# Kernel optimization log

Measured on AMD Instinct MI355X. Metric: run time of the kernel, lower is better.

## Reference

```python
import jax, jax.numpy as jnp
import numpy as np

B, N, M, D = 4096, 50, 64, 64   # batch, fields_dim, embedding_dim, product_layer_dim
V = 100000                      # features_dim (vocab)
HIDDEN = [512, 256, 128]
BN_EPS = 1e-3


def setup_inputs() -> dict:
    key = jax.random.key(0)
    ks = jax.random.split(key, 32)
    inp = {
        "feature_value": jax.random.uniform(ks[0], (B, N), dtype=jnp.float32),
        "embedding_index": jax.random.randint(ks[1], (B, N), 0, V, dtype=jnp.int32),
        "emb_table": jax.random.uniform(ks[2], (V, M), dtype=jnp.float32, minval=-0.05, maxval=0.05),
        "linear_signals": jax.random.normal(ks[3], (D, N, M), dtype=jnp.float32) * 0.05,
        "theta": jax.random.normal(ks[4], (D, N), dtype=jnp.float32) * 0.05,
        "quad_w": jax.random.normal(ks[5], (D, M, M), dtype=jnp.float32) * 0.05,
    }
    in_dim = 3 * D  # concat(l_z, l_p_inner, l_p_outer)
    dims = [in_dim] + HIDDEN
    k = 6
    for i, (di, do) in enumerate(zip(dims[:-1], dims[1:])):
        inp[f"W{i}"] = jax.random.normal(ks[k], (di, do), dtype=jnp.float32) * (1.0 / np.sqrt(di)); k += 1
        inp[f"b{i}"] = jnp.zeros((do,), dtype=jnp.float32)
        inp[f"g{i}"] = jnp.ones((do,), dtype=jnp.float32)
        inp[f"be{i}"] = jnp.zeros((do,), dtype=jnp.float32)
        inp[f"m{i}"] = jnp.zeros((do,), dtype=jnp.float32)
        inp[f"v{i}"] = jnp.ones((do,), dtype=jnp.float32)
    inp["Wout"] = jax.random.normal(ks[k], (HIDDEN[-1], 1), dtype=jnp.float32) * (1.0 / np.sqrt(HIDDEN[-1]))
    inp["bout"] = jnp.zeros((1,), dtype=jnp.float32)
    return inp


def _pnn_forward(feature_value, embedding_index, emb_table, linear_signals, theta, quad_w,
                 dense_params, Wout, bout):
    # features: [b, n, m] = embedding lookup scaled per-field by feature_value
    feats = emb_table[embedding_index] * feature_value[:, :, None]
    # linear signal: 'bnm,dnm->bd'
    l_z = jnp.einsum('bnm,dnm->bd', feats, linear_signals)
    # ipnn branch: delta = 'dn,bnm->bdnm'; l_p = sum delta*delta over (n,m)
    # algebraic rewrite (same math): sum_n theta_dn^2 * (sum_m feats_bnm^2)
    l_p_in = jnp.einsum('bn,dn->bd', jnp.sum(feats * feats, axis=2), theta * theta)
    # opnn branch: p = outer(sum_feats, sum_feats); 'bmn,dmn->bd'
    s = jnp.sum(feats, axis=1)  # [b, m]
    l_p_out = jnp.einsum('bm,dmn,bn->bd', s, quad_w, s)
    x = jnp.concatenate([l_z, l_p_in, l_p_out], axis=1)  # [b, 3d]
    # MLP stack: Dense -> BatchNorm(inference) -> ReLU (dropout is identity at eval)
    for (W, b, g, be, mu, var) in dense_params:
        x = x @ W + b
        x = g * (x - mu) * jax.lax.rsqrt(var + BN_EPS) + be
        x = jax.nn.relu(x)
    return jax.nn.sigmoid(x @ Wout + bout)


def reference(feature_value, embedding_index, emb_table, linear_signals, theta, quad_w,
              W0, b0, g0, be0, m0, v0,
              W1, b1, g1, be1, m1, v1,
              W2, b2, g2, be2, m2, v2,
              Wout, bout):
    dense_params = [(W0, b0, g0, be0, m0, v0),
                    (W1, b1, g1, be1, m1, v1),
                    (W2, b2, g2, be2, m2, v2)]
    return _pnn_forward(feature_value, embedding_index, emb_table, linear_signals, theta,
                        quad_w, dense_params, Wout, bout)
```

## Files before the change

### kernel.cpp

```cpp
#include <hip/hip_runtime.h>
#include <hip/hip_bf16.h>
#include <math.h>

#define B 4096
#define NF 50
#define BN_EPS 1e-3f
#define ROWS 16

typedef float f32x4 __attribute__((ext_vector_type(4)));
typedef __bf16 bf16x8 __attribute__((ext_vector_type(8)));
#define MFMA __builtin_amdgcn_mfma_f32_16x16x32_bf16

__device__ __forceinline__ unsigned short f2b(float x) {
  unsigned u = __float_as_uint(x);
  return (unsigned short)((u + 0x7FFFu + ((u >> 16) & 1u)) >> 16);
}
__device__ __forceinline__ unsigned packbf(float a, float b) {
  return ((unsigned)f2b(b) << 16) | (unsigned)f2b(a);
}
__device__ __forceinline__ float bs2f(unsigned short u) {
  return __uint_as_float(((unsigned)u) << 16);
}

#define WS_LS  0
#define WS_QW  204800
#define WS_W0  466944
#define WS_W1  565248
#define WS_W2  696320

__global__ __launch_bounds__(256) void prep(
    const float* __restrict__ ls, const float* __restrict__ qw,
    const float* __restrict__ W0, const float* __restrict__ W1,
    const float* __restrict__ W2, unsigned short* __restrict__ ws)
{
  int bid = blockIdx.x, t = threadIdx.x;
  if (bid < 228) {
    int o = (bid * 256 + t) * 8;
    const float* src = (o < 204800) ? (ls + o) : (qw + (o - 204800));
    float4 a = *(const float4*)src, b = *(const float4*)(src + 4);
    int4 v = {(int)packbf(a.x, a.y), (int)packbf(a.z, a.w),
              (int)packbf(b.x, b.y), (int)packbf(b.z, b.w)};
    *(int4*)&ws[o] = v;
    return;
  }
  __shared__ unsigned short sh[64 * 72];
  int id = bid - 228;
  const float* W; int K, Ncols, kt, nt, wofs;
  if (id < 24)      { W = W0; K = 192; Ncols = 512; kt = id >> 3; nt = id & 7;  wofs = WS_W0; }
  else if (id < 56) { int j = id - 24; W = W1; K = 512; Ncols = 256; kt = j >> 2; nt = j & 3; wofs = WS_W1; }
  else              { int j = id - 56; W = W2; K = 256; Ncols = 128; kt = j >> 1; nt = j & 1; wofs = WS_W2; }
  int k0 = kt * 64, n0 = nt * 64;
  {
    int r = t >> 2, cs = (t & 3) * 16;
    const float* src = W + (size_t)(k0 + r) * Ncols + n0 + cs;
    float4 a = *(const float4*)src, b = *(const float4*)(src + 4);
    float4 c = *(const float4*)(src + 8), d = *(const float4*)(src + 12);
    unsigned short* dst = &sh[r * 72 + cs];
    *(int4*)dst = int4{(int)packbf(a.x, a.y), (int)packbf(a.z, a.w),
                       (int)packbf(b.x, b.y), (int)packbf(b.z, b.w)};
    *(int4*)(dst + 8) = int4{(int)packbf(c.x, c.y), (int)packbf(c.z, c.w),
                             (int)packbf(d.x, d.y), (int)packbf(d.z, d.w)};
  }
  __syncthreads();
  {
    int nr = t >> 2, ks = (t & 3) * 16;
    unsigned short vbuf[16];
#pragma unroll
    for (int j = 0; j < 16; ++j) vbuf[j] = sh[(ks + j) * 72 + nr];
    unsigned short* dst = &ws[wofs + (size_t)(n0 + nr) * K + k0 + ks];
    *(int4*)dst = *(int4*)&vbuf[0];
    *(int4*)(dst + 8) = *(int4*)&vbuf[8];
  }
}

__global__ __launch_bounds__(512) void pnn_main(
    const float* __restrict__ fv, const int* __restrict__ idx,
    const float* __restrict__ emb, const float* __restrict__ theta,
    const unsigned short* __restrict__ ws,
    const float* __restrict__ b0p, const float* __restrict__ g0p,
    const float* __restrict__ be0p, const float* __restrict__ m0p,
    const float* __restrict__ v0p,
    const float* __restrict__ b1p, const float* __restrict__ g1p,
    const float* __restrict__ be1p, const float* __restrict__ m1p,
    const float* __restrict__ v1p,
    const float* __restrict__ b2p, const float* __restrict__ g2p,
    const float* __restrict__ be2p, const float* __restrict__ m2p,
    const float* __restrict__ v2p,
    const float* __restrict__ Wout, const float* __restrict__ boutp,
    float* __restrict__ out)
{
  __shared__ unsigned short feats[25 * 16 * 136];
  __shared__ int   idx_s[ROWS * NF];
  __shared__ float fv_s[ROWS * NF];
  __shared__ float th2_s[64 * NF];
  __shared__ float s_s[ROWS * 68];
  __shared__ float sq_s[ROWS * 64];
  __shared__ unsigned short x_s[ROWS * 200];

  unsigned short* h0_s = feats;
  unsigned short* h1_s = feats + 8320;
  unsigned short* h2_s = feats + 12544;

  const unsigned short* lsb = ws + WS_LS;
  const unsigned short* qwb = ws + WS_QW;
  const unsigned short* w0t = ws + WS_W0;
  const unsigned short* w1t = ws + WS_W1;
  const unsigned short* w2t = ws + WS_W2;

  const int t    = threadIdx.x;
  const int w    = t >> 6;
  const int l    = t & 63;
  const int m16  = l & 15;
  const int qoff = (l >> 4) * 8;
  const int b0   = blockIdx.x * ROWS;

  for (int i = t; i < ROWS * NF; i += 512) {
    idx_s[i] = idx[b0 * NF + i];
    fv_s[i]  = fv[b0 * NF + i];
  }
  for (int i = t; i < 64 * NF; i += 512) { float v = theta[i]; th2_s[i] = v * v; }
  __syncthreads();

  {
    const int row = t >> 5;
    const int m2  = (t & 31) * 2;
    float s0 = 0.f, s1 = 0.f;
    for (int g = 0; g < 5; ++g) {
      float2 e[10];
#pragma unroll
      for (int j = 0; j < 5; ++j) {
        int n0 = (g * 5 + j) * 2;
        int iv0 = idx_s[row * NF + n0], iv1 = idx_s[row * NF + n0 + 1];
        e[2 * j]     = *(const float2*)(emb + (size_t)iv0 * 64 + m2);
        e[2 * j + 1] = *(const float2*)(emb + (size_t)iv1 * 64 + m2);
      }
#pragma unroll
      for (int j = 0; j < 5; ++j) {
        int c = g * 5 + j;
        int n0 = 2 * c, n1 = n0 + 1;
        float f0 = fv_s[row * NF + n0], f1 = fv_s[row * NF + n1];
        float p00 = f0 * e[2 * j].x,     p01 = f0 * e[2 * j].y;
        float p10 = f1 * e[2 * j + 1].x, p11 = f1 * e[2 * j + 1].y;
        unsigned short* fc = feats + c * 2176 + row * 136;
        *(unsigned*)&fc[m2]      = packbf(p00, p01);
        *(unsigned*)&fc[64 + m2] = packbf(p10, p11);
        s0 += p00 + p10; s1 += p01 + p11;
        float q0 = p00 * p00 + p01 * p01;
        float q1 = p10 * p10 + p11 * p11;
        q0 += __shfl_xor(q0, 16); q0 += __shfl_xor(q0, 8); q0 += __shfl_xor(q0, 4);
        q0 += __shfl_xor(q0, 2);  q0 += __shfl_xor(q0, 1);
        q1 += __shfl_xor(q1, 16); q1 += __shfl_xor(q1, 8); q1 += __shfl_xor(q1, 4);
        q1 += __shfl_xor(q1, 2);  q1 += __shfl_xor(q1, 1);
        if ((t & 31) == 0) { sq_s[row * 64 + n0] = q0; sq_s[row * 64 + n1] = q1; }
      }
    }
    float2 sv; sv.x = s0; sv.y = s1;
    *(float2*)&s_s[row * 68 + m2] = sv;
  }
  __syncthreads();

  if (w < 4) {
    const int dt = w;
    f32x4 a0v = {0.f, 0.f, 0.f, 0.f}, a1v = {0.f, 0.f, 0.f, 0.f};
    const unsigned short* lp0 = lsb + (size_t)(dt * 16 + m16) * 3200 + qoff;
    const int arow = m16 * 136 + qoff;
    for (int g = 0; g < 5; ++g) {
      bf16x8 bv[20];
#pragma unroll
      for (int cc = 0; cc < 5; ++cc) {
        const unsigned short* lp = lp0 + (g * 5 + cc) * 128;
#pragma unroll
        for (int s4 = 0; s4 < 4; ++s4)
          bv[cc * 4 + s4] = *(const bf16x8*)(lp + s4 * 32);
      }
#pragma unroll
      for (int cc = 0; cc < 5; ++cc) {
        const unsigned short* fc = feats + (g * 5 + cc) * 2176 + arow;
#pragma unroll
        for (int s4 = 0; s4 < 4; ++s4) {
          bf16x8 av = *(const bf16x8*)(fc + s4 * 32);
          if (s4 & 1) a1v = MFMA(av, bv[cc * 4 + s4], a1v, 0, 0, 0);
          else        a0v = MFMA(av, bv[cc * 4 + s4], a0v, 0, 0, 0);
        }
      }
    }
#pragma unroll
    for (int r = 0; r < 4; ++r)
      x_s[((l >> 4) * 4 + r) * 200 + dt * 16 + m16] = f2b(a0v[r] + a1v[r]);
    {
      int d = dt * 16 + m16;
      float acc[4] = {0.f, 0.f, 0.f, 0.f};
      for (int n = 0; n < NF; ++n) {
        float th2 = th2_s[d * NF + n];
#pragma unroll
        for (int r = 0; r < 4; ++r)
          acc[r] += sq_s[((l >> 4) * 4 + r) * 64 + n] * th2;
      }
#pragma unroll
      for (int r = 0; r < 4; ++r)
        x_s[((l >> 4) * 4 + r) * 200 + 64 + d] = f2b(acc[r]);
    }
  } else {
    const int dt = w - 4;
    const int row = m16;
    const int nb = qoff;
    float sn[16];
    *(float4*)&sn[0]  = *(const float4*)&s_s[row * 68 + nb];
    *(float4*)&sn[4]  = *(const float4*)&s_s[row * 68 + nb + 4];
    *(float4*)&sn[8]  = *(const float4*)&s_s[row * 68 + 32 + nb];
    *(float4*)&sn[12] = *(const float4*)&s_s[row * 68 + 32 + nb + 4];
    f32x4 a0v = {0.f, 0.f, 0.f, 0.f}, a1v = {0.f, 0.f, 0.f, 0.f};
    const unsigned short* qp0 = qwb + (size_t)(dt * 16 + m16) * 4096 + qoff;
    for (int g = 0; g < 8; ++g) {
      bf16x8 bv[16];
#pragma unroll
      for (int mi = 0; mi < 8; ++mi) {
        const unsigned short* qp = qp0 + (g * 8 + mi) * 64;
        bv[2 * mi]     = *(const bf16x8*)qp;
        bv[2 * mi + 1] = *(const bf16x8*)(qp + 32);
      }
#pragma unroll
      for (int mi = 0; mi < 8; ++mi) {
        float sm = s_s[row * 68 + g * 8 + mi];
        union { unsigned u[4]; bf16x8 v; } af0, af1;
#pragma unroll
        for (int j = 0; j < 4; ++j) {
          af0.u[j] = packbf(sm * sn[2 * j],     sm * sn[2 * j + 1]);
          af1.u[j] = packbf(sm * sn[8 + 2 * j], sm * sn[8 + 2 * j + 1]);
        }
        a0v = MFMA(af0.v, bv[2 * mi],     a0v, 0, 0, 0);
        a1v = MFMA(af1.v, bv[2 * mi + 1], a1v, 0, 0, 0);
      }
    }
#pragma unroll
    for (int r = 0; r < 4; ++r)
      x_s[((l >> 4) * 4 + r) * 200 + 128 + dt * 16 + m16] = f2b(a0v[r] + a1v[r]);
  }
  __syncthreads();

  {
    int ar = m16 * 200 + qoff;
    bf16x8 xa[6];
#pragma unroll
    for (int kc = 0; kc < 6; ++kc) xa[kc] = *(const bf16x8*)&x_s[ar + kc * 32];
    for (int j = 0; j < 4; ++j) {
      int n0 = (w * 4 + j) * 16;
      const unsigned short* wp = w0t + (size_t)(n0 + m16) * 192 + qoff;
      bf16x8 bv[6];
#pragma unroll
      for (int kc = 0; kc < 6; ++kc) bv[kc] = *(const bf16x8*)(wp + kc * 32);
      f32x4 ha = {0.f, 0.f, 0.f, 0.f}, hb = {0.f, 0.f, 0.f, 0.f};
#pragma unroll
      for (int kc = 0; kc < 6; ++kc) {
        if (kc & 1) hb = MFMA(xa[kc], bv[kc], hb, 0, 0, 0);
        else        ha = MFMA(xa[kc], bv[kc], ha, 0, 0, 0);
      }
      int n = n0 + m16;
      float sc = g0p[n] * rsqrtf(v0p[n] + BN_EPS);
      float sh = be0p[n] + (b0p[n] - m0p[n]) * sc;
#pragma unroll
      for (int r = 0; r < 4; ++r) {
        float v = fmaxf((ha[r] + hb[r]) * sc + sh, 0.f);
        h0_s[((l >> 4) * 4 + r) * 520 + n] = f2b(v);
      }
    }
  }
  __syncthreads();

  for (int j = 0; j < 2; ++j) {
    int n0 = (w * 2 + j) * 16;
    const unsigned short* wp = w1t + (size_t)(n0 + m16) * 512 + qoff;
    bf16x8 bv[16];
#pragma unroll
    for (int kc = 0; kc < 16; ++kc) bv[kc] = *(const bf16x8*)(wp + kc * 32);
    int ar = m16 * 520 + qoff;
    f32x4 ha = {0.f, 0.f, 0.f, 0.f}, hb = {0.f, 0.f, 0.f, 0.f};
#pragma unroll
    for (int kc = 0; kc < 16; ++kc) {
      bf16x8 av = *(const bf16x8*)&h0_s[ar + kc * 32];
      if (kc & 1) hb = MFMA(av, bv[kc], hb, 0, 0, 0);
      else        ha = MFMA(av, bv[kc], ha, 0, 0, 0);
    }
    int n = n0 + m16;
    float sc = g1p[n] * rsqrtf(v1p[n] + BN_EPS);
    float sh = be1p[n] + (b1p[n] - m1p[n]) * sc;
#pragma unroll
    for (int r = 0; r < 4; ++r) {
      float v = fmaxf((ha[r] + hb[r]) * sc + sh, 0.f);
      h1_s[((l >> 4) * 4 + r) * 264 + n] = f2b(v);
    }
  }
  __syncthreads();

  {
    int n0 = w * 16;
    const unsigned short* wp = w2t + (size_t)(n0 + m16) * 256 + qoff;
    bf16x8 bv[8];
#pragma unroll
    for (int kc = 0; kc < 8; ++kc) bv[kc] = *(const bf16x8*)(wp + kc * 32);
    int ar = m16 * 264 + qoff;
    f32x4 ha = {0.f, 0.f, 0.f, 0.f}, hb = {0.f, 0.f, 0.f, 0.f};
#pragma unroll
    for (int kc = 0; kc < 8; ++kc) {
      bf16x8 av = *(const bf16x8*)&h1_s[ar + kc * 32];
      if (kc & 1) hb = MFMA(av, bv[kc], hb, 0, 0, 0);
      else        ha = MFMA(av, bv[kc], ha, 0, 0, 0);
    }
    int n = n0 + m16;
    float sc = g2p[n] * rsqrtf(v2p[n] + BN_EPS);
    float sh = be2p[n] + (b2p[n] - m2p[n]) * sc;
#pragma unroll
    for (int r = 0; r < 4; ++r) {
      float v = fmaxf((ha[r] + hb[r]) * sc + sh, 0.f);
      h2_s[((l >> 4) * 4 + r) * 136 + n] = f2b(v);
    }
  }
  __syncthreads();

  if (t < 128) {
    int bb = t >> 3, seg = t & 7;
    float a = 0.f;
#pragma unroll
    for (int j = 0; j < 16; ++j) {
      int k = seg * 16 + j;
      a += bs2f(h2_s[bb * 136 + k]) * Wout[k];
    }
    a += __shfl_xor(a, 4); a += __shfl_xor(a, 2); a += __shfl_xor(a, 1);
    if (seg == 0) out[b0 + bb] = 1.f / (1.f + expf(-(a + boutp[0])));
  }
}

extern "C" void kernel_launch(void* const* d_in, const int* in_sizes, int n_in,
                              void* d_out, int out_size, void* d_ws, size_t ws_size,
                              hipStream_t stream)
{
  (void)in_sizes; (void)n_in; (void)out_size; (void)ws_size;
  unsigned short* ws = (unsigned short*)d_ws;

  prep<<<292, 256, 0, stream>>>(
      (const float*)d_in[3], (const float*)d_in[5], (const float*)d_in[6],
      (const float*)d_in[12], (const float*)d_in[18], ws);

  pnn_main<<<B / ROWS, 512, 0, stream>>>(
      (const float*)d_in[0], (const int*)d_in[1], (const float*)d_in[2],
      (const float*)d_in[4], ws,
      (const float*)d_in[7],  (const float*)d_in[8],  (const float*)d_in[9],
      (const float*)d_in[10], (const float*)d_in[11],
      (const float*)d_in[13], (const float*)d_in[14], (const float*)d_in[15],
      (const float*)d_in[16], (const float*)d_in[17],
      (const float*)d_in[19], (const float*)d_in[20], (const float*)d_in[21],
      (const float*)d_in[22], (const float*)d_in[23],
      (const float*)d_in[24], (const float*)d_in[25],
      (float*)d_out);
}
```

Measured before the change: 172.6 us.

## Double block size to 1024 threads and split-K the product-layer MFMAs

Launches 16 waves per block instead of 8. Each wave gathers one batch row's embeddings. The linear and outer-product GEMMs are split along K across wave pairs, with partial sums reduced through new shared buffers. The inner-product term moves into a separate reduction step using a transposed theta^2 table, and the MLP layer work is redistributed across the extra waves. This aims to raise latency hiding and per-block parallelism, at the cost of more LDS, an extra barrier, and register pressure under launch bounds of 1024.

```diff
diff --git a/kernel.cpp b/kernel.cpp
--- a/kernel.cpp
+++ b/kernel.cpp
@@ -73,7 +73,7 @@
   }
 }
 
-__global__ __launch_bounds__(512) void pnn_main(
+__global__ __launch_bounds__(1024, 4) void pnn_main(
     const float* __restrict__ fv, const int* __restrict__ idx,
     const float* __restrict__ emb, const float* __restrict__ theta,
     const unsigned short* __restrict__ ws,
@@ -92,9 +92,11 @@
   __shared__ unsigned short feats[25 * 16 * 136];
   __shared__ int   idx_s[ROWS * NF];
   __shared__ float fv_s[ROWS * NF];
-  __shared__ float th2_s[64 * NF];
+  __shared__ float th2t_s[NF * 64];
   __shared__ float s_s[ROWS * 68];
   __shared__ float sq_s[ROWS * 64];
+  __shared__ float redA[2 * ROWS * 66];
+  __shared__ float redB[2 * ROWS * 66];
   __shared__ unsigned short x_s[ROWS * 200];
 
   unsigned short* h0_s = feats;
@@ -114,94 +116,109 @@
   const int qoff = (l >> 4) * 8;
   const int b0   = blockIdx.x * ROWS;
 
-  for (int i = t; i < ROWS * NF; i += 512) {
+  for (int i = t; i < ROWS * NF; i += 1024) {
     idx_s[i] = idx[b0 * NF + i];
     fv_s[i]  = fv[b0 * NF + i];
   }
-  for (int i = t; i < 64 * NF; i += 512) { float v = theta[i]; th2_s[i] = v * v; }
-  __syncthreads();
-
-  {
-    const int row = t >> 5;
-    const int m2  = (t & 31) * 2;
+  for (int i = t; i < NF * 64; i += 1024) {
+    int n = i >> 6, d = i & 63;
+    float v = theta[d * NF + n];
+    th2t_s[i] = v * v;
+  }
+  __syncthreads();
+
+  {
+    const int row = w;
+    const int p   = l >> 5;
+    const int m2  = (l & 31) * 2;
+    const int base = row * NF;
     float s0 = 0.f, s1 = 0.f;
-    for (int g = 0; g < 5; ++g) {
-      float2 e[10];
-#pragma unroll
-      for (int j = 0; j < 5; ++j) {
-        int n0 = (g * 5 + j) * 2;
-        int iv0 = idx_s[row * NF + n0], iv1 = idx_s[row * NF + n0 + 1];
-        e[2 * j]     = *(const float2*)(emb + (size_t)iv0 * 64 + m2);
-        e[2 * j + 1] = *(const float2*)(emb + (size_t)iv1 * 64 + m2);
-      }
-#pragma unroll
-      for (int j = 0; j < 5; ++j) {
-        int c = g * 5 + j;
-        int n0 = 2 * c, n1 = n0 + 1;
-        float f0 = fv_s[row * NF + n0], f1 = fv_s[row * NF + n1];
-        float p00 = f0 * e[2 * j].x,     p01 = f0 * e[2 * j].y;
-        float p10 = f1 * e[2 * j + 1].x, p11 = f1 * e[2 * j + 1].y;
-        unsigned short* fc = feats + c * 2176 + row * 136;
-        *(unsigned*)&fc[m2]      = packbf(p00, p01);
-        *(unsigned*)&fc[64 + m2] = packbf(p10, p11);
-        s0 += p00 + p10; s1 += p01 + p11;
-        float q0 = p00 * p00 + p01 * p01;
-        float q1 = p10 * p10 + p11 * p11;
-        q0 += __shfl_xor(q0, 16); q0 += __shfl_xor(q0, 8); q0 += __shfl_xor(q0, 4);
-        q0 += __shfl_xor(q0, 2);  q0 += __shfl_xor(q0, 1);
-        q1 += __shfl_xor(q1, 16); q1 += __shfl_xor(q1, 8); q1 += __shfl_xor(q1, 4);
-        q1 += __shfl_xor(q1, 2);  q1 += __shfl_xor(q1, 1);
-        if ((t & 31) == 0) { sq_s[row * 64 + n0] = q0; sq_s[row * 64 + n1] = q1; }
-      }
-    }
-    float2 sv; sv.x = s0; sv.y = s1;
-    *(float2*)&s_s[row * 68 + m2] = sv;
-  }
-  __syncthreads();
-
-  if (w < 4) {
-    const int dt = w;
+    {
+      float2 e[13];
+#pragma unroll
+      for (int j = 0; j < 13; ++j) {
+        int iv = idx_s[base + 2 * j + p];
+        e[j] = *(const float2*)(emb + (size_t)iv * 64 + m2);
+      }
+#pragma unroll
+      for (int j = 0; j < 13; ++j) {
+        int n = 2 * j + p;
+        float fvv = fv_s[base + n];
+        float p0 = fvv * e[j].x, p1 = fvv * e[j].y;
+        *(unsigned*)&feats[j * 2176 + row * 136 + p * 64 + m2] = packbf(p0, p1);
+        s0 += p0; s1 += p1;
+        float q = p0 * p0 + p1 * p1;
+        q += __shfl_xor(q, 16); q += __shfl_xor(q, 8); q += __shfl_xor(q, 4);
+        q += __shfl_xor(q, 2);  q += __shfl_xor(q, 1);
+        if ((l & 31) == 0) sq_s[row * 64 + n] = q;
+      }
+    }
+    {
+      float2 e[12];
+#pragma unroll
+      for (int j = 13; j < 25; ++j) {
+        int iv = idx_s[base + 2 * j + p];
+        e[j - 13] = *(const float2*)(emb + (size_t)iv * 64 + m2);
+      }
+#pragma unroll
+      for (int j = 13; j < 25; ++j) {
+        int n = 2 * j + p;
+        float fvv = fv_s[base + n];
+        float p0 = fvv * e[j - 13].x, p1 = fvv * e[j - 13].y;
+        *(unsigned*)&feats[j * 2176 + row * 136 + p * 64 + m2] = packbf(p0, p1);
+        s0 += p0; s1 += p1;
+        float q = p0 * p0 + p1 * p1;
+        q += __shfl_xor(q, 16); q += __shfl_xor(q, 8); q += __shfl_xor(q, 4);
+        q += __shfl_xor(q, 2);  q += __shfl_xor(q, 1);
+        if ((l & 31) == 0) sq_s[row * 64 + n] = q;
+      }
+    }
+    s0 += __shfl_xor(s0, 32);
+    s1 += __shfl_xor(s1, 32);
+    if (l < 32) {
+      float2 sv; sv.x = s0; sv.y = s1;
+      *(float2*)&s_s[row * 68 + m2] = sv;
+    }
+  }
+  __syncthreads();
+
+  if (w < 8) {
+    const int dt = w >> 1, kh = w & 1;
+    const int c0 = kh ? 13 : 0, c1 = kh ? 25 : 13;
     f32x4 a0v = {0.f, 0.f, 0.f, 0.f}, a1v = {0.f, 0.f, 0.f, 0.f};
     const unsigned short* lp0 = lsb + (size_t)(dt * 16 + m16) * 3200 + qoff;
     const int arow = m16 * 136 + qoff;
-    for (int g = 0; g < 5; ++g) {
-      bf16x8 bv[20];
-#pragma unroll
-      for (int cc = 0; cc < 5; ++cc) {
-        const unsigned short* lp = lp0 + (g * 5 + cc) * 128;
-#pragma unroll
-        for (int s4 = 0; s4 < 4; ++s4)
-          bv[cc * 4 + s4] = *(const bf16x8*)(lp + s4 * 32);
-      }
-#pragma unroll
-      for (int cc = 0; cc < 5; ++cc) {
-        const unsigned short* fc = feats + (g * 5 + cc) * 2176 + arow;
-#pragma unroll
-        for (int s4 = 0; s4 < 4; ++s4) {
-          bf16x8 av = *(const bf16x8*)(fc + s4 * 32);
-          if (s4 & 1) a1v = MFMA(av, bv[cc * 4 + s4], a1v, 0, 0, 0);
-          else        a0v = MFMA(av, bv[cc * 4 + s4], a0v, 0, 0, 0);
+    for (int cg = c0; cg < c1; cg += 4) {
+      bf16x8 bv[16];
+#pragma unroll
+      for (int u = 0; u < 4; ++u) {
+        int cc = cg + u;
+        if (cc < c1) {
+          const unsigned short* lp = lp0 + cc * 128;
+#pragma unroll
+          for (int s4 = 0; s4 < 4; ++s4)
+            bv[u * 4 + s4] = *(const bf16x8*)(lp + s4 * 32);
         }
       }
+#pragma unroll
+      for (int u = 0; u < 4; ++u) {
+        int cc = cg + u;
+        if (cc < c1) {
+          const unsigned short* fc = feats + cc * 2176 + arow;
+#pragma unroll
+          for (int s4 = 0; s4 < 4; ++s4) {
+            bf16x8 av = *(const bf16x8*)(fc + s4 * 32);
+            if (s4 & 1) a1v = MFMA(av, bv[u * 4 + s4], a1v, 0, 0, 0);
+            else        a0v = MFMA(av, bv[u * 4 + s4], a0v, 0, 0, 0);
+          }
+        }
+      }
     }
 #pragma unroll
     for (int r = 0; r < 4; ++r)
-      x_s[((l >> 4) * 4 + r) * 200 + dt * 16 + m16] = f2b(a0v[r] + a1v[r]);
-    {
-      int d = dt * 16 + m16;
-      float acc[4] = {0.f, 0.f, 0.f, 0.f};
-      for (int n = 0; n < NF; ++n) {
-        float th2 = th2_s[d * NF + n];
-#pragma unroll
-        for (int r = 0; r < 4; ++r)
-          acc[r] += sq_s[((l >> 4) * 4 + r) * 64 + n] * th2;
-      }
-#pragma unroll
-      for (int r = 0; r < 4; ++r)
-        x_s[((l >> 4) * 4 + r) * 200 + 64 + d] = f2b(acc[r]);
-    }
+      redA[kh * 1056 + ((l >> 4) * 4 + r) * 66 + dt * 16 + m16] = a0v[r] + a1v[r];
   } else {
-    const int dt = w - 4;
+    const int dt = (w - 8) >> 1, kh = w & 1;
     const int row = m16;
     const int nb = qoff;
     float sn[16];
@@ -211,17 +228,18 @@
     *(float4*)&sn[12] = *(const float4*)&s_s[row * 68 + 32 + nb + 4];
     f32x4 a0v = {0.f, 0.f, 0.f, 0.f}, a1v = {0.f, 0.f, 0.f, 0.f};
     const unsigned short* qp0 = qwb + (size_t)(dt * 16 + m16) * 4096 + qoff;
-    for (int g = 0; g < 8; ++g) {
+    for (int g = 0; g < 4; ++g) {
       bf16x8 bv[16];
 #pragma unroll
       for (int mi = 0; mi < 8; ++mi) {
-        const unsigned short* qp = qp0 + (g * 8 + mi) * 64;
+        int mm = kh * 32 + g * 8 + mi;
+        const unsigned short* qp = qp0 + mm * 64;
         bv[2 * mi]     = *(const bf16x8*)qp;
         bv[2 * mi + 1] = *(const bf16x8*)(qp + 32);
       }
 #pragma unroll
       for (int mi = 0; mi < 8; ++mi) {
-        float sm = s_s[row * 68 + g * 8 + mi];
+        float sm = s_s[row * 68 + kh * 32 + g * 8 + mi];
         union { unsigned u[4]; bf16x8 v; } af0, af1;
 #pragma unroll
         for (int j = 0; j < 4; ++j) {
@@ -234,7 +252,19 @@
     }
 #pragma unroll
     for (int r = 0; r < 4; ++r)
-      x_s[((l >> 4) * 4 + r) * 200 + 128 + dt * 16 + m16] = f2b(a0v[r] + a1v[r]);
+      redB[kh * 1056 + ((l >> 4) * 4 + r) * 66 + dt * 16 + m16] = a0v[r] + a1v[r];
+  }
+  __syncthreads();
+
+  {
+    float lz = redA[w * 66 + l] + redA[1056 + w * 66 + l];
+    x_s[w * 200 + l] = f2b(lz);
+    float lp = redB[w * 66 + l] + redB[1056 + w * 66 + l];
+    x_s[w * 200 + 128 + l] = f2b(lp);
+    float a = 0.f;
+    for (int n = 0; n < NF; ++n)
+      a += sq_s[w * 64 + n] * th2t_s[n * 64 + l];
+    x_s[w * 200 + 64 + l] = f2b(a);
   }
   __syncthreads();
 
@@ -243,8 +273,8 @@
     bf16x8 xa[6];
 #pragma unroll
     for (int kc = 0; kc < 6; ++kc) xa[kc] = *(const bf16x8*)&x_s[ar + kc * 32];
-    for (int j = 0; j < 4; ++j) {
-      int n0 = (w * 4 + j) * 16;
+    for (int j = 0; j < 2; ++j) {
+      int n0 = (w * 2 + j) * 16;
       const unsigned short* wp = w0t + (size_t)(n0 + m16) * 192 + qoff;
       bf16x8 bv[6];
 #pragma unroll
@@ -267,8 +297,8 @@
   }
   __syncthreads();
 
-  for (int j = 0; j < 2; ++j) {
-    int n0 = (w * 2 + j) * 16;
+  {
+    int n0 = w * 16;
     const unsigned short* wp = w1t + (size_t)(n0 + m16) * 512 + qoff;
     bf16x8 bv[16];
 #pragma unroll
@@ -292,7 +322,7 @@
   }
   __syncthreads();
 
-  {
+  if (w < 8) {
     int n0 = w * 16;
     const unsigned short* wp = w2t + (size_t)(n0 + m16) * 256 + qoff;
     bf16x8 bv[8];
@@ -341,7 +371,7 @@
       (const float*)d_in[3], (const float*)d_in[5], (const float*)d_in[6],
       (const float*)d_in[12], (const float*)d_in[18], ws);
 
-  pnn_main<<<B / ROWS, 512, 0, stream>>>(
+  pnn_main<<<B / ROWS, 1024, 0, stream>>>(
       (const float*)d_in[0], (const int*)d_in[1], (const float*)d_in[2],
       (const float*)d_in[4], ws,
       (const float*)d_in[7],  (const float*)d_in[8],  (const float*)d_in[9],
```

Result: no change. 174.3 us (+1.0%).
